# Performance work log

Measured on AMD Instinct MI355X. Metric: run time of the kernel, lower is better.

Reference implementation:

```python
import jax, jax.numpy as jnp
import numpy as np

CONCENTRATION_WEIGHT = 1.0


def setup_inputs() -> dict:
    key = jax.random.key(0)
    k1, k2 = jax.random.split(key)
    pred = jax.random.normal(k1, (16, 10, 512, 512), dtype=jnp.float32)
    target = jax.random.uniform(k2, (16, 10, 512, 512), dtype=jnp.float32)
    return {"pred": pred, "target": target}


def reference(pred, target):
    # pred, target: [B, C, H, W]
    B, C, H, W = pred.shape
    y = jnp.arange(H, dtype=pred.dtype)[:, None]   # [H,1]
    x = jnp.arange(W, dtype=pred.dtype)[None, :]   # [1,W]

    mass = target.sum(axis=(2, 3))                 # [B,C]
    valid = mass > 0                               # [B,C] bool
    safe_mass = jnp.where(valid, mass, jnp.ones_like(mass))

    # masked centroids per (b,c)
    cy = (target * y).sum(axis=(2, 3)) / safe_mass  # [B,C]
    cx = (target * x).sum(axis=(2, 3)) / safe_mass  # [B,C]

    # squared distance field per (b,c): [B,C,H,W]
    dist_sq = (y[None, None, :, :] - cy[:, :, None, None]) ** 2 \
            + (x[None, None, :, :] - cx[:, :, None, None]) ** 2

    per_slice = jnp.mean(jax.nn.sigmoid(pred) * dist_sq, axis=(2, 3))  # [B,C]

    n_valid = valid.sum()
    loss_sum = jnp.where(valid, per_slice, jnp.zeros_like(per_slice)).sum()
    loss = jnp.where(n_valid > 0,
                     loss_sum / jnp.maximum(n_valid, 1).astype(pred.dtype),
                     jnp.asarray(0.0, dtype=pred.dtype))
    return loss * CONCENTRATION_WEIGHT
```

## Files before the change

### kernel.cpp

```cpp
#include <hip/hip_runtime.h>


#define BB 16
#define CC 10
#define HH 512
#define WW 512
#define HW (HH * WW)
#define SLICES (BB * CC)
#define CHUNKS 16
#define V4_PER_CHUNK (HW / CHUNKS / 4)
#define THREADS 256
#define V4_PER_THREAD (V4_PER_CHUNK / THREADS)
#define NACC 8

__global__ __launch_bounds__(THREADS) void conc_pass1(
    const float* __restrict__ pred,
    const float* __restrict__ target,
    float* __restrict__ ws) {
  const int slice = blockIdx.x / CHUNKS;
  const int chunk = blockIdx.x % CHUNKS;
  const int tid = threadIdx.x;

  const float4* __restrict__ p4 =
      reinterpret_cast<const float4*>(pred + (size_t)slice * HW) + chunk * V4_PER_CHUNK;
  const float4* __restrict__ t4 =
      reinterpret_cast<const float4*>(target + (size_t)slice * HW) + chunk * V4_PER_CHUNK;

  float tm = 0.f, ty = 0.f, tx = 0.f;
  float s0 = 0.f, sy = 0.f, sx = 0.f, syy = 0.f, sxx = 0.f;

#pragma unroll
  for (int i = 0; i < V4_PER_THREAD; ++i) {
    const int v = i * THREADS + tid;
    const float4 t = t4[v];
    const float4 p = p4[v];
    const int e = (chunk * V4_PER_CHUNK + v) * 4;
    const float y  = (float)(e >> 9);
    const float x0 = (float)(e & 511);
    const float x1 = x0 + 1.f, x2 = x0 + 2.f, x3 = x0 + 3.f;

    const float tsum = (t.x + t.y) + (t.z + t.w);
    tm += tsum;
    ty += tsum * y;
    tx += t.x * x0 + t.y * x1 + t.z * x2 + t.w * x3;

    const float g0 = 1.f / (1.f + __expf(-p.x));
    const float g1 = 1.f / (1.f + __expf(-p.y));
    const float g2 = 1.f / (1.f + __expf(-p.z));
    const float g3 = 1.f / (1.f + __expf(-p.w));
    const float gs = (g0 + g1) + (g2 + g3);
    s0  += gs;
    sy  += gs * y;
    syy += gs * (y * y);
    const float gx = g0 * x0 + g1 * x1 + g2 * x2 + g3 * x3;
    sx  += gx;
    sxx += g0 * (x0 * x0) + g1 * (x1 * x1) + g2 * (x2 * x2) + g3 * (x3 * x3);
  }

  float acc[NACC] = {tm, ty, tx, s0, sy, sx, syy, sxx};
#pragma unroll
  for (int k = 0; k < NACC; ++k) {
    float v = acc[k];
#pragma unroll
    for (int off = 32; off > 0; off >>= 1) v += __shfl_down(v, off, 64);
    acc[k] = v;
  }
  __shared__ float red[4][NACC];
  const int lane = tid & 63, wave = tid >> 6;
  if (lane == 0) {
#pragma unroll
    for (int k = 0; k < NACC; ++k) red[wave][k] = acc[k];
  }
  __syncthreads();
  if (tid == 0) {
    float* out = ws + (size_t)blockIdx.x * NACC;
#pragma unroll
    for (int k = 0; k < NACC; ++k)
      out[k] = red[0][k] + red[1][k] + red[2][k] + red[3][k];
  }
}

__global__ __launch_bounds__(THREADS) void conc_pass2(
    const float* __restrict__ ws, float* __restrict__ out) {
  const int tid = threadIdx.x;
  double lsum = 0.0;
  int nvalid = 0;

  for (int s = tid; s < SLICES; s += THREADS) {
    float a[NACC];
#pragma unroll
    for (int k = 0; k < NACC; ++k) a[k] = 0.f;
    for (int c = 0; c < CHUNKS; ++c) {
      const float* p = ws + (size_t)(s * CHUNKS + c) * NACC;
#pragma unroll
      for (int k = 0; k < NACC; ++k) a[k] += p[k];
    }
    const double tm = a[0], ty = a[1], tx = a[2];
    const double s0 = a[3], sy = a[4], sx = a[5], syy = a[6], sxx = a[7];
    const bool valid = tm > 0.0;
    const double mass = valid ? tm : 1.0;
    const double cy = ty / mass, cx = tx / mass;
    const double conc =
        syy + sxx - 2.0 * cy * sy - 2.0 * cx * sx + (cy * cy + cx * cx) * s0;
    if (valid) {
      lsum += conc / (double)HW;
      ++nvalid;
    }
  }

  __shared__ double sd[THREADS];
  __shared__ int si[THREADS];
  sd[tid] = lsum;
  si[tid] = nvalid;
  __syncthreads();
  for (int off = THREADS / 2; off > 0; off >>= 1) {
    if (tid < off) {
      sd[tid] += sd[tid + off];
      si[tid] += si[tid + off];
    }
    __syncthreads();
  }
  if (tid == 0) {
    const double loss = (si[0] > 0) ? (sd[0] / (double)si[0]) : 0.0;
    out[0] = (float)loss;
  }
}

extern "C" void kernel_launch(void* const* d_in, const int* in_sizes, int n_in,
                              void* d_out, int out_size, void* d_ws, size_t ws_size,
                              hipStream_t stream) {
  const float* pred = (const float*)d_in[0];
  const float* target = (const float*)d_in[1];
  float* ws = (float*)d_ws;
  float* out = (float*)d_out;

  conc_pass1<<<SLICES * CHUNKS, THREADS, 0, stream>>>(pred, target, ws);
  conc_pass2<<<1, THREADS, 0, stream>>>(ws, out);
}
```

Measured before the change: 65.44 us.

## Split slices into more chunks, batch loads, and parallelize final reduction per wave

Pass 1 is templated on the chunk count. When the workspace is large enough it launches 64 chunks per slice instead of 16, giving 10240 blocks. The inner loop now issues four float4 loads of each input before computing on them, which raises memory-level parallelism. Pass 2 gives each of 8 waves one slice at a time, reducing chunk partials with wave shuffles instead of one thread looping serially, at the cost of a larger workspace and more partials to combine.

```diff
diff --git a/kernel.cpp b/kernel.cpp
--- a/kernel.cpp
+++ b/kernel.cpp
@@ -7,54 +7,62 @@
 #define WW 512
 #define HW (HH * WW)
 #define SLICES (BB * CC)
-#define CHUNKS 16
-#define V4_PER_CHUNK (HW / CHUNKS / 4)
 #define THREADS 256
-#define V4_PER_THREAD (V4_PER_CHUNK / THREADS)
 #define NACC 8
 
+template <int CH>
 __global__ __launch_bounds__(THREADS) void conc_pass1(
     const float* __restrict__ pred,
     const float* __restrict__ target,
     float* __restrict__ ws) {
-  const int slice = blockIdx.x / CHUNKS;
-  const int chunk = blockIdx.x % CHUNKS;
+  constexpr int V4C = HW / 4 / CH;
+  constexpr int VPT = V4C / THREADS;
+  const int slice = blockIdx.x / CH;
+  const int chunk = blockIdx.x % CH;
   const int tid = threadIdx.x;
 
   const float4* __restrict__ p4 =
-      reinterpret_cast<const float4*>(pred + (size_t)slice * HW) + chunk * V4_PER_CHUNK;
+      reinterpret_cast<const float4*>(pred + (size_t)slice * HW) + chunk * V4C;
   const float4* __restrict__ t4 =
-      reinterpret_cast<const float4*>(target + (size_t)slice * HW) + chunk * V4_PER_CHUNK;
+      reinterpret_cast<const float4*>(target + (size_t)slice * HW) + chunk * V4C;
 
   float tm = 0.f, ty = 0.f, tx = 0.f;
   float s0 = 0.f, sy = 0.f, sx = 0.f, syy = 0.f, sxx = 0.f;
 
+  for (int b = 0; b < VPT; b += 4) {
+    float4 tb[4], pb[4];
 #pragma unroll
-  for (int i = 0; i < V4_PER_THREAD; ++i) {
-    const int v = i * THREADS + tid;
-    const float4 t = t4[v];
-    const float4 p = p4[v];
-    const int e = (chunk * V4_PER_CHUNK + v) * 4;
-    const float y  = (float)(e >> 9);
-    const float x0 = (float)(e & 511);
-    const float x1 = x0 + 1.f, x2 = x0 + 2.f, x3 = x0 + 3.f;
+    for (int j = 0; j < 4; ++j) {
+      const int v = (b + j) * THREADS + tid;
+      tb[j] = t4[v];
+      pb[j] = p4[v];
+    }
+#pragma unroll
+    for (int j = 0; j < 4; ++j) {
+      const int v = (b + j) * THREADS + tid;
+      const int e = (chunk * V4C + v) * 4;
+      const float y  = (float)(e >> 9);
+      const float x0 = (float)(e & 511);
+      const float x1 = x0 + 1.f, x2 = x0 + 2.f, x3 = x0 + 3.f;
+      const float4 t = tb[j];
+      const float4 p = pb[j];
 
-    const float tsum = (t.x + t.y) + (t.z + t.w);
-    tm += tsum;
-    ty += tsum * y;
-    tx += t.x * x0 + t.y * x1 + t.z * x2 + t.w * x3;
+      const float tsum = (t.x + t.y) + (t.z + t.w);
+      tm += tsum;
+      ty += tsum * y;
+      tx += t.x * x0 + t.y * x1 + t.z * x2 + t.w * x3;
 
-    const float g0 = 1.f / (1.f + __expf(-p.x));
-    const float g1 = 1.f / (1.f + __expf(-p.y));
-    const float g2 = 1.f / (1.f + __expf(-p.z));
-    const float g3 = 1.f / (1.f + __expf(-p.w));
-    const float gs = (g0 + g1) + (g2 + g3);
-    s0  += gs;
-    sy  += gs * y;
-    syy += gs * (y * y);
-    const float gx = g0 * x0 + g1 * x1 + g2 * x2 + g3 * x3;
-    sx  += gx;
-    sxx += g0 * (x0 * x0) + g1 * (x1 * x1) + g2 * (x2 * x2) + g3 * (x3 * x3);
+      const float g0 = 1.f / (1.f + __expf(-p.x));
+      const float g1 = 1.f / (1.f + __expf(-p.y));
+      const float g2 = 1.f / (1.f + __expf(-p.z));
+      const float g3 = 1.f / (1.f + __expf(-p.w));
+      const float gs = (g0 + g1) + (g2 + g3);
+      s0  += gs;
+      sy  += gs * y;
+      syy += gs * (y * y);
+      sx  += g0 * x0 + g1 * x1 + g2 * x2 + g3 * x3;
+      sxx += g0 * (x0 * x0) + g1 * (x1 * x1) + g2 * (x2 * x2) + g3 * (x3 * x3);
+    }
   }
 
   float acc[NACC] = {tm, ty, tx, s0, sy, sx, syy, sxx};
@@ -80,49 +88,65 @@
   }
 }
 
-__global__ __launch_bounds__(THREADS) void conc_pass2(
+template <int CH>
+__global__ __launch_bounds__(512) void conc_pass2(
     const float* __restrict__ ws, float* __restrict__ out) {
   const int tid = threadIdx.x;
+  const int lane = tid & 63, wave = tid >> 6;
+
   double lsum = 0.0;
   int nvalid = 0;
 
-  for (int s = tid; s < SLICES; s += THREADS) {
-    float a[NACC];
+  for (int s = wave; s < SLICES; s += 8) {
+    float m[NACC];
+    if (lane < CH) {
+      const float4* r =
+          reinterpret_cast<const float4*>(ws + ((size_t)s * CH + lane) * NACC);
+      const float4 a = r[0], b = r[1];
+      m[0] = a.x; m[1] = a.y; m[2] = a.z; m[3] = a.w;
+      m[4] = b.x; m[5] = b.y; m[6] = b.z; m[7] = b.w;
+    } else {
 #pragma unroll
-    for (int k = 0; k < NACC; ++k) a[k] = 0.f;
-    for (int c = 0; c < CHUNKS; ++c) {
-      const float* p = ws + (size_t)(s * CHUNKS + c) * NACC;
+      for (int k = 0; k < NACC; ++k) m[k] = 0.f;
+    }
 #pragma unroll
-      for (int k = 0; k < NACC; ++k) a[k] += p[k];
+    for (int k = 0; k < NACC; ++k) {
+      float v = m[k];
+#pragma unroll
+      for (int off = 32; off > 0; off >>= 1) v += __shfl_xor(v, off, 64);
+      m[k] = v;
     }
-    const double tm = a[0], ty = a[1], tx = a[2];
-    const double s0 = a[3], sy = a[4], sx = a[5], syy = a[6], sxx = a[7];
-    const bool valid = tm > 0.0;
-    const double mass = valid ? tm : 1.0;
-    const double cy = ty / mass, cx = tx / mass;
-    const double conc =
-        syy + sxx - 2.0 * cy * sy - 2.0 * cx * sx + (cy * cy + cx * cx) * s0;
-    if (valid) {
-      lsum += conc / (double)HW;
-      ++nvalid;
+    if (lane == 0) {
+      const double tm = m[0], ty = m[1], tx = m[2];
+      const double s0 = m[3], sy = m[4], sx = m[5], syy = m[6], sxx = m[7];
+      const bool valid = tm > 0.0;
+      const double mass = valid ? tm : 1.0;
+      const double cy = ty / mass, cx = tx / mass;
+      const double conc =
+          syy + sxx - 2.0 * cy * sy - 2.0 * cx * sx + (cy * cy + cx * cx) * s0;
+      if (valid) {
+        lsum += conc / (double)HW;
+        ++nvalid;
+      }
     }
   }
 
-  __shared__ double sd[THREADS];
-  __shared__ int si[THREADS];
-  sd[tid] = lsum;
-  si[tid] = nvalid;
+  __shared__ double sd[8];
+  __shared__ int si[8];
+  if (lane == 0) {
+    sd[wave] = lsum;
+    si[wave] = nvalid;
+  }
   __syncthreads();
-  for (int off = THREADS / 2; off > 0; off >>= 1) {
-    if (tid < off) {
-      sd[tid] += sd[tid + off];
-      si[tid] += si[tid + off];
+  if (tid == 0) {
+    double t = 0.0;
+    int n = 0;
+#pragma unroll
+    for (int w = 0; w < 8; ++w) {
+      t += sd[w];
+      n += si[w];
     }
-    __syncthreads();
-  }
-  if (tid == 0) {
-    const double loss = (si[0] > 0) ? (sd[0] / (double)si[0]) : 0.0;
-    out[0] = (float)loss;
+    out[0] = (float)((n > 0) ? (t / (double)n) : 0.0);
   }
 }
 
@@ -134,6 +158,12 @@
   float* ws = (float*)d_ws;
   float* out = (float*)d_out;
 
-  conc_pass1<<<SLICES * CHUNKS, THREADS, 0, stream>>>(pred, target, ws);
-  conc_pass2<<<1, THREADS, 0, stream>>>(ws, out);
+  const size_t need64 = (size_t)SLICES * 64 * NACC * sizeof(float);
+  if (ws_size >= need64) {
+    conc_pass1<64><<<SLICES * 64, THREADS, 0, stream>>>(pred, target, ws);
+    conc_pass2<64><<<1, 512, 0, stream>>>(ws, out);
+  } else {
+    conc_pass1<16><<<SLICES * 16, THREADS, 0, stream>>>(pred, target, ws);
+    conc_pass2<16><<<1, 512, 0, stream>>>(ws, out);
+  }
 }
```

Measured after the change: 83.84 us. 1.28x slower.

## Rebalance pass1 grid to one full wave with slice-straddling blocks

Applied to the files above, without the earlier changes.

Reshapes the reduction grid from 2560 slice-aligned chunks to 2048 equal blocks of 5120 float4, sized to fill the device in a single wave. Blocks that cross a slice boundary flush two partial records, which pass2 gathers per slice. Loads are batched four at a time per group, and the final reduction uses wave shuffles instead of a shared-memory tree. The cost targeted is the partial tail wave; the trade is extra barriers and branching for boundary blocks.

```diff
diff --git a/kernel.cpp b/kernel.cpp
--- a/kernel.cpp
+++ b/kernel.cpp
@@ -1,82 +1,106 @@
 #include <hip/hip_runtime.h>
 
 
-#define BB 16
-#define CC 10
-#define HH 512
-#define WW 512
-#define HW (HH * WW)
-#define SLICES (BB * CC)
-#define CHUNKS 16
-#define V4_PER_CHUNK (HW / CHUNKS / 4)
+#define HW 262144
+#define F4_SLICE 65536
+#define SLICES 160
+#define NBLK 2048
+#define V4B 5120
+#define GROUPS 5
 #define THREADS 256
-#define V4_PER_THREAD (V4_PER_CHUNK / THREADS)
 #define NACC 8
 
-__global__ __launch_bounds__(THREADS) void conc_pass1(
+__global__ __launch_bounds__(THREADS, 8) void conc_pass1(
     const float* __restrict__ pred,
     const float* __restrict__ target,
     float* __restrict__ ws) {
-  const int slice = blockIdx.x / CHUNKS;
-  const int chunk = blockIdx.x % CHUNKS;
+  const int b = blockIdx.x;
   const int tid = threadIdx.x;
+  const int start4 = b * V4B;
 
-  const float4* __restrict__ p4 =
-      reinterpret_cast<const float4*>(pred + (size_t)slice * HW) + chunk * V4_PER_CHUNK;
-  const float4* __restrict__ t4 =
-      reinterpret_cast<const float4*>(target + (size_t)slice * HW) + chunk * V4_PER_CHUNK;
+  const float4* __restrict__ p4 = reinterpret_cast<const float4*>(pred);
+  const float4* __restrict__ t4 = reinterpret_cast<const float4*>(target);
 
   float tm = 0.f, ty = 0.f, tx = 0.f;
   float s0 = 0.f, sy = 0.f, sx = 0.f, syy = 0.f, sxx = 0.f;
 
+  __shared__ float red[4][NACC];
+  const int lane = tid & 63, wave = tid >> 6;
+
+  auto flush = [&](int rec) {
+    float acc[NACC] = {tm, ty, tx, s0, sy, sx, syy, sxx};
 #pragma unroll
-  for (int i = 0; i < V4_PER_THREAD; ++i) {
-    const int v = i * THREADS + tid;
-    const float4 t = t4[v];
-    const float4 p = p4[v];
-    const int e = (chunk * V4_PER_CHUNK + v) * 4;
-    const float y  = (float)(e >> 9);
-    const float x0 = (float)(e & 511);
-    const float x1 = x0 + 1.f, x2 = x0 + 2.f, x3 = x0 + 3.f;
+    for (int k = 0; k < NACC; ++k) {
+      float v = acc[k];
+#pragma unroll
+      for (int off = 32; off > 0; off >>= 1) v += __shfl_down(v, off, 64);
+      acc[k] = v;
+    }
+    if (lane == 0) {
+#pragma unroll
+      for (int k = 0; k < NACC; ++k) red[wave][k] = acc[k];
+    }
+    __syncthreads();
+    if (tid < NACC)
+      ws[(size_t)(b * 2 + rec) * NACC + tid] =
+          red[0][tid] + red[1][tid] + red[2][tid] + red[3][tid];
+    __syncthreads();
+  };
 
-    const float tsum = (t.x + t.y) + (t.z + t.w);
-    tm += tsum;
-    ty += tsum * y;
-    tx += t.x * x0 + t.y * x1 + t.z * x2 + t.w * x3;
+  const int s0b = start4 >> 16;
+  const int off_in_slice = start4 & (F4_SLICE - 1);
+  const bool crosses = (off_in_slice + V4B) > F4_SLICE;
+  const int cg = crosses ? ((F4_SLICE - off_in_slice) >> 10) : GROUPS;
 
-    const float g0 = 1.f / (1.f + __expf(-p.x));
-    const float g1 = 1.f / (1.f + __expf(-p.y));
-    const float g2 = 1.f / (1.f + __expf(-p.z));
-    const float g3 = 1.f / (1.f + __expf(-p.w));
-    const float gs = (g0 + g1) + (g2 + g3);
-    s0  += gs;
-    sy  += gs * y;
-    syy += gs * (y * y);
-    const float gx = g0 * x0 + g1 * x1 + g2 * x2 + g3 * x3;
-    sx  += gx;
-    sxx += g0 * (x0 * x0) + g1 * (x1 * x1) + g2 * (x2 * x2) + g3 * (x3 * x3);
+  bool flushed = false;
+#pragma unroll
+  for (int g = 0; g < GROUPS; ++g) {
+    if (g == cg) {
+      flush(0);
+      flushed = true;
+      tm = ty = tx = s0 = sy = sx = syy = sxx = 0.f;
+    }
+    const int g4 = start4 + g * 1024;
+    float4 tb[4], pb[4];
+#pragma unroll
+    for (int k = 0; k < 4; ++k) {
+      const int v4 = g4 + k * THREADS + tid;
+      tb[k] = t4[v4];
+      pb[k] = p4[v4];
+    }
+#pragma unroll
+    for (int k = 0; k < 4; ++k) {
+      const int v4 = g4 + k * THREADS + tid;
+      const int e = (v4 & (F4_SLICE - 1)) << 2;
+      const float y  = (float)(e >> 9);
+      const float x0 = (float)(e & 511);
+      const float x1 = x0 + 1.f, x2 = x0 + 2.f, x3 = x0 + 3.f;
+      const float4 t = tb[k];
+      const float4 p = pb[k];
+
+      const float tsum = (t.x + t.y) + (t.z + t.w);
+      tm += tsum;
+      ty += tsum * y;
+      tx += t.x * x0 + t.y * x1 + t.z * x2 + t.w * x3;
+
+      const float g0 = 1.f / (1.f + __expf(-p.x));
+      const float g1 = 1.f / (1.f + __expf(-p.y));
+      const float g2 = 1.f / (1.f + __expf(-p.z));
+      const float g3 = 1.f / (1.f + __expf(-p.w));
+      const float gs = (g0 + g1) + (g2 + g3);
+      s0  += gs;
+      sy  += gs * y;
+      syy += gs * (y * y);
+      sx  += g0 * x0 + g1 * x1 + g2 * x2 + g3 * x3;
+      sxx += g0 * (x0 * x0) + g1 * (x1 * x1) + g2 * (x2 * x2) + g3 * (x3 * x3);
+    }
   }
 
-  float acc[NACC] = {tm, ty, tx, s0, sy, sx, syy, sxx};
-#pragma unroll
-  for (int k = 0; k < NACC; ++k) {
-    float v = acc[k];
-#pragma unroll
-    for (int off = 32; off > 0; off >>= 1) v += __shfl_down(v, off, 64);
-    acc[k] = v;
-  }
-  __shared__ float red[4][NACC];
-  const int lane = tid & 63, wave = tid >> 6;
-  if (lane == 0) {
-#pragma unroll
-    for (int k = 0; k < NACC; ++k) red[wave][k] = acc[k];
-  }
-  __syncthreads();
-  if (tid == 0) {
-    float* out = ws + (size_t)blockIdx.x * NACC;
-#pragma unroll
-    for (int k = 0; k < NACC; ++k)
-      out[k] = red[0][k] + red[1][k] + red[2][k] + red[3][k];
+  if (flushed) {
+    flush(1);
+  } else {
+    flush(0);
+    if (tid < NACC) ws[(size_t)(b * 2 + 1) * NACC + tid] = 0.f;
   }
 }
 
@@ -86,43 +110,51 @@
   double lsum = 0.0;
   int nvalid = 0;
 
-  for (int s = tid; s < SLICES; s += THREADS) {
+  if (tid < SLICES) {
+    const int s = tid;
     float a[NACC];
 #pragma unroll
     for (int k = 0; k < NACC; ++k) a[k] = 0.f;
-    for (int c = 0; c < CHUNKS; ++c) {
-      const float* p = ws + (size_t)(s * CHUNKS + c) * NACC;
+
+    const int blo = (s * F4_SLICE) / V4B;
+    const int bhi = ((s + 1) * F4_SLICE - 1) / V4B;
+    for (int b = blo; b <= bhi; ++b) {
+      const int s0b = (b * V4B) >> 16;
+      const int rec = (s0b == s) ? 0 : 1;
+      const float* r = ws + (size_t)(b * 2 + rec) * NACC;
 #pragma unroll
-      for (int k = 0; k < NACC; ++k) a[k] += p[k];
+      for (int k = 0; k < NACC; ++k) a[k] += r[k];
     }
+
     const double tm = a[0], ty = a[1], tx = a[2];
-    const double s0 = a[3], sy = a[4], sx = a[5], syy = a[6], sxx = a[7];
+    const double m0 = a[3], msy = a[4], msx = a[5], syy = a[6], sxx = a[7];
     const bool valid = tm > 0.0;
     const double mass = valid ? tm : 1.0;
     const double cy = ty / mass, cx = tx / mass;
     const double conc =
-        syy + sxx - 2.0 * cy * sy - 2.0 * cx * sx + (cy * cy + cx * cx) * s0;
+        syy + sxx - 2.0 * cy * msy - 2.0 * cx * msx + (cy * cy + cx * cx) * m0;
     if (valid) {
       lsum += conc / (double)HW;
-      ++nvalid;
+      nvalid = 1;
     }
   }
 
-  __shared__ double sd[THREADS];
-  __shared__ int si[THREADS];
-  sd[tid] = lsum;
-  si[tid] = nvalid;
+  const int lane = tid & 63, wave = tid >> 6;
+  double v = lsum;
+  int n = nvalid;
+#pragma unroll
+  for (int off = 32; off > 0; off >>= 1) {
+    v += __shfl_down(v, off, 64);
+    n += __shfl_down(n, off, 64);
+  }
+  __shared__ double sd[4];
+  __shared__ int si[4];
+  if (lane == 0) { sd[wave] = v; si[wave] = n; }
   __syncthreads();
-  for (int off = THREADS / 2; off > 0; off >>= 1) {
-    if (tid < off) {
-      sd[tid] += sd[tid + off];
-      si[tid] += si[tid + off];
-    }
-    __syncthreads();
-  }
   if (tid == 0) {
-    const double loss = (si[0] > 0) ? (sd[0] / (double)si[0]) : 0.0;
-    out[0] = (float)loss;
+    double t = sd[0] + sd[1] + sd[2] + sd[3];
+    int nn = si[0] + si[1] + si[2] + si[3];
+    out[0] = (float)((nn > 0) ? (t / (double)nn) : 0.0);
   }
 }
 
@@ -134,6 +166,6 @@
   float* ws = (float*)d_ws;
   float* out = (float*)d_out;
 
-  conc_pass1<<<SLICES * CHUNKS, THREADS, 0, stream>>>(pred, target, ws);
+  conc_pass1<<<NBLK, THREADS, 0, stream>>>(pred, target, ws);
   conc_pass2<<<1, THREADS, 0, stream>>>(ws, out);
 }
```

After: 97.25 us. +48.6%, slower.
